# Kernel tuning notes

Measured on AMD Instinct MI355X. Metric: run time of the kernel, lower is better.

## Reference

```python
import jax, jax.numpy as jnp
import numpy as np

N_NODES = 50000
N_EDGES = 400000
D_IN = 2048
D_OUT = 512


def setup_inputs() -> dict:
    key = jax.random.key(0)
    k1, k2, k3 = jax.random.split(key, 3)
    x = jax.random.normal(k1, (N_NODES, D_IN), dtype=jnp.float32)
    edge_index = jax.random.randint(k2, (2, N_EDGES), 0, N_NODES, dtype=jnp.int64)
    # Glorot init like PyG GCNConv
    scale = jnp.sqrt(6.0 / (D_IN + D_OUT)).astype(jnp.float32)
    weight = jax.random.uniform(k3, (D_IN, D_OUT), dtype=jnp.float32, minval=-scale, maxval=scale)
    bias = jnp.zeros((D_OUT,), dtype=jnp.float32)
    return {"x": x, "edge_index": edge_index, "weight": weight, "bias": bias}


def reference(x, edge_index, weight, bias):
    N = x.shape[0]
    # GCNConv(normalize=True): add self-loops, symmetric deg^-1/2 normalization
    loops = jnp.arange(N, dtype=edge_index.dtype)
    src = jnp.concatenate([edge_index[0], loops])  # message sources (x_j)
    dst = jnp.concatenate([edge_index[1], loops])  # aggregation targets
    ones = jnp.ones(dst.shape[0], dtype=x.dtype)
    deg = jax.ops.segment_sum(ones, dst, num_segments=N)  # [N]
    deg_inv_sqrt = jnp.where(deg > 0, jax.lax.rsqrt(deg), 0.0)
    norm = deg_inv_sqrt[src] * deg_inv_sqrt[dst]  # [E+N]
    h = x @ weight  # [N, d_out] linear transform before propagation
    msgs = norm[:, None] * h[src]  # [E+N, d_out]
    out = jax.ops.segment_sum(msgs, dst, num_segments=N) + bias  # [N, d_out]
    return jax.nn.log_softmax(out, axis=1)
```

## Files before the change

### kernel.cpp

```cpp
#include <hip/hip_runtime.h>
#include <stdint.h>

#define D_IN   2048
#define D_OUT  512

typedef __bf16 bf16;
typedef bf16     bf16x8 __attribute__((ext_vector_type(8)));
typedef float    f32x4  __attribute__((ext_vector_type(4)));
typedef uint32_t u32x4  __attribute__((ext_vector_type(4)));

#define GLP(p)  (const __attribute__((address_space(1))) void*)(p)
#define LDSP(p) (__attribute__((address_space(3))) void*)(p)

__global__ void k_count(const int* __restrict__ dstv, int* __restrict__ cnt, int E) {
    int e = blockIdx.x * blockDim.x + threadIdx.x;
    if (e < E) atomicAdd(&cnt[dstv[e]], 1);
}

__global__ __launch_bounds__(1024) void k_scan1(const int* __restrict__ cnt,
                                                int* __restrict__ offs,
                                                int* __restrict__ bsum,
                                                float* __restrict__ dis,
                                                int* __restrict__ cur, int n) {
    __shared__ int wsum[16], wbase[16];
    const int tid = threadIdx.x, lane = tid & 63, wv = tid >> 6;
    int i = blockIdx.x * 1024 + tid;
    int v = (i < n) ? cnt[i] : 0;
    int x = v;
    #pragma unroll
    for (int d = 1; d < 64; d <<= 1) {
        int y = __shfl_up(x, d);
        if (lane >= d) x += y;
    }
    if (lane == 63) wsum[wv] = x;
    __syncthreads();
    if (tid < 16) {
        int s = 0;
        for (int j = 0; j < tid; ++j) s += wsum[j];
        wbase[tid] = s;
    }
    __syncthreads();
    if (i < n) {
        offs[i] = wbase[wv] + x - v;
        dis[i]  = rsqrtf((float)(v + 1));
        cur[i]  = 0;
    }
    if (tid == 0) bsum[blockIdx.x] = wbase[15] + wsum[15];
}

__global__ void k_scan2(int* __restrict__ bsum, int nb) {
    int t = threadIdx.x;
    if (nb <= 64) {
        int v = (t < nb) ? bsum[t] : 0;
        int x = v;
        #pragma unroll
        for (int d = 1; d < 64; d <<= 1) {
            int y = __shfl_up(x, d);
            if (t >= d) x += y;
        }
        if (t < nb) bsum[t] = x - v;
    } else if (t == 0) {
        int run = 0;
        for (int j = 0; j < nb; ++j) { int v = bsum[j]; bsum[j] = run; run += v; }
    }
}

__global__ void k_fill(const int* __restrict__ srcv, const int* __restrict__ dstv,
                       const int* __restrict__ offs, const int* __restrict__ bsum,
                       int* __restrict__ cur, int* __restrict__ csr, int E) {
    int e = blockIdx.x * blockDim.x + threadIdx.x;
    if (e < E) {
        int d = dstv[e];
        int p = offs[d] + bsum[d >> 10] + atomicAdd(&cur[d], 1);
        csr[p] = srcv[e];
    }
}

__global__ void k_wt(const float* __restrict__ W, uint16_t* __restrict__ wt) {
    __shared__ float t[32][33];
    int kb = blockIdx.x * 32, nb = blockIdx.y * 32;
    int tx = threadIdx.x, ty = threadIdx.y;
    #pragma unroll
    for (int i = 0; i < 32; i += 8)
        t[ty + i][tx] = W[(size_t)(kb + ty + i) * D_OUT + nb + tx];
    __syncthreads();
    bf16* o = (bf16*)wt;
    #pragma unroll
    for (int i = 0; i < 32; i += 8)
        o[(size_t)(nb + ty + i) * D_IN + kb + tx] = (bf16)t[tx][ty + i];
}

__global__ __launch_bounds__(256, 2) void k_gemm(const float* __restrict__ X,
                                                 const uint16_t* __restrict__ WT,
                                                 uint16_t* __restrict__ H, int M) {
    __shared__ uint16_t lsA[2][128 * 64];
    __shared__ uint16_t lsB[2][128 * 64];
    const int nwg = gridDim.x;
    const int b = blockIdx.x;
    const int q = nwg >> 3, r = nwg & 7;
    const int xcd = b & 7, lo = b >> 3;
    const int g = (xcd < r) ? (xcd * (q + 1) + lo) : (r * (q + 1) + (xcd - r) * q + lo);
    const int m0 = (g >> 2) * 128;
    const int n0 = (g & 3) * 128;
    const int tid = threadIdx.x;
    const int w = tid >> 6, lane = tid & 63;
    const int wr = w >> 1, wc = w & 1;
    const int lr = lane & 15, lk = lane >> 4;
    const int NT = D_IN / 64;

    f32x4 acc[4][4];
    #pragma unroll
    for (int m = 0; m < 4; m++)
        #pragma unroll
        for (int n = 0; n < 4; n++) acc[m][n] = (f32x4)(0.0f);

    const float* aSrc[4];
    int aDst[4];
    const uint16_t* bSrc[4];
    #pragma unroll
    for (int j = 0; j < 4; j++) {
        int uidx = (w * 4 + j) * 64 + lane;
        int row = uidx >> 3, u = uidx & 7;
        int lrow = row;
        if (m0 + row >= M) lrow = (M - 1) - m0;
        aSrc[j] = X + (size_t)(m0 + lrow) * D_IN + u * 8;
        aDst[j] = row * 64 + (u ^ (row & 7)) * 8;
        bSrc[j] = WT + (size_t)(n0 + row) * D_IN + (u ^ (row & 7)) * 8;
    }

    f32x4 set0[8], set1[8];

    auto loadA = [&](f32x4* s, int t) {
        t &= (NT - 1);
        #pragma unroll
        for (int j = 0; j < 4; j++) {
            s[2 * j]     = *(const f32x4*)(aSrc[j] + t * 64);
            s[2 * j + 1] = *(const f32x4*)(aSrc[j] + t * 64 + 4);
        }
    };
    auto writeA = [&](const f32x4* s, int buf) {
        #pragma unroll
        for (int j = 0; j < 4; j++) {
            f32x4 a0 = s[2 * j], a1 = s[2 * j + 1];
            bf16x8 tv;
            tv[0] = (bf16)a0[0]; tv[1] = (bf16)a0[1]; tv[2] = (bf16)a0[2]; tv[3] = (bf16)a0[3];
            tv[4] = (bf16)a1[0]; tv[5] = (bf16)a1[1]; tv[6] = (bf16)a1[2]; tv[7] = (bf16)a1[3];
            *(bf16x8*)(&lsA[buf][aDst[j]]) = tv;
        }
    };
    auto stageB = [&](int t, int buf) {
        t &= (NT - 1);
        #pragma unroll
        for (int j = 0; j < 4; j++)
            __builtin_amdgcn_global_load_lds(GLP(bSrc[j] + t * 64),
                                             LDSP(&lsB[buf][(w * 4 + j) * 512]), 16, 0, 0);
    };
    auto compute = [&](int buf) {
        #pragma unroll
        for (int kk = 0; kk < 2; kk++) {
            bf16x8 aF[4], bF[4];
            #pragma unroll
            for (int m = 0; m < 4; m++) {
                int row = wr * 64 + m * 16 + lr;
                aF[m] = *(const bf16x8*)(&lsA[buf][row * 64 + (((kk * 4 + lk) ^ (row & 7)) * 8)]);
            }
            #pragma unroll
            for (int n = 0; n < 4; n++) {
                int row = wc * 64 + n * 16 + lr;
                bF[n] = *(const bf16x8*)(&lsB[buf][row * 64 + (((kk * 4 + lk) ^ (row & 7)) * 8)]);
            }
            #pragma unroll
            for (int m = 0; m < 4; m++)
                #pragma unroll
                for (int n = 0; n < 4; n++)
                    acc[m][n] = __builtin_amdgcn_mfma_f32_16x16x32_bf16(aF[m], bF[n], acc[m][n], 0, 0, 0);
        }
    };

    loadA(set0, 0);
    stageB(0, 0);
    loadA(set1, 1);
    asm volatile("s_waitcnt vmcnt(12)" ::: "memory");
    writeA(set0, 0);

    #pragma unroll 1
    for (int t = 0; t < NT; t += 2) {
        stageB(t + 1, 1);
        loadA(set0, t + 2);
        asm volatile("s_waitcnt vmcnt(12)" ::: "memory");
        writeA(set1, 1);
        asm volatile("s_waitcnt lgkmcnt(0)" ::: "memory");
        __builtin_amdgcn_s_barrier();
        compute(0);
        __builtin_amdgcn_s_barrier();
        stageB(t + 2, 0);
        loadA(set1, t + 3);
        asm volatile("s_waitcnt vmcnt(12)" ::: "memory");
        writeA(set0, 0);
        asm volatile("s_waitcnt lgkmcnt(0)" ::: "memory");
        __builtin_amdgcn_s_barrier();
        compute(1);
        __builtin_amdgcn_s_barrier();
    }
    asm volatile("s_waitcnt vmcnt(0)" ::: "memory");

    #pragma unroll
    for (int m = 0; m < 4; m++) {
        int rbase = m0 + wr * 64 + m * 16 + lk * 4;
        #pragma unroll
        for (int n = 0; n < 4; n++) {
            int col = n0 + wc * 64 + n * 16 + lr;
            #pragma unroll
            for (int j = 0; j < 4; j++) {
                int row = rbase + j;
                if (row < M) {
                    bf16 tv = (bf16)acc[m][n][j];
                    H[(size_t)row * D_OUT + col] = __builtin_bit_cast(uint16_t, tv);
                }
            }
        }
    }
}

__global__ __launch_bounds__(256) void k_agg(const uint16_t* __restrict__ h,
                                             const int* __restrict__ csr,
                                             const int* __restrict__ offs,
                                             const int* __restrict__ bsum,
                                             const int* __restrict__ cnt,
                                             const float* __restrict__ dis,
                                             const float* __restrict__ bias,
                                             float* __restrict__ out, int N) {
    const int wv = threadIdx.x >> 6, lane = threadIdx.x & 63;
    const int i = blockIdx.x * 4 + wv;
    if (i >= N) return;
    const float di = dis[i];
    float acc[8];
    {
        u32x4 v = *(const u32x4*)(h + (size_t)i * D_OUT + lane * 8);
        float s2 = di * di;
        #pragma unroll
        for (int k = 0; k < 4; k++) {
            acc[2 * k]     = __builtin_bit_cast(float, v[k] << 16) * s2;
            acc[2 * k + 1] = __builtin_bit_cast(float, v[k] & 0xffff0000u) * s2;
        }
    }
    const int o = offs[i] + bsum[i >> 10], c = cnt[i];
    for (int e = o; e < o + c; ++e) {
        int s = csr[e];
        float ws = di * dis[s];
        u32x4 v = *(const u32x4*)(h + (size_t)s * D_OUT + lane * 8);
        #pragma unroll
        for (int k = 0; k < 4; k++) {
            acc[2 * k]     += __builtin_bit_cast(float, v[k] << 16) * ws;
            acc[2 * k + 1] += __builtin_bit_cast(float, v[k] & 0xffff0000u) * ws;
        }
    }
    {
        const f32x4* bp = (const f32x4*)(bias + lane * 8);
        f32x4 b0 = bp[0], b1 = bp[1];
        #pragma unroll
        for (int k = 0; k < 4; k++) { acc[k] += b0[k]; acc[4 + k] += b1[k]; }
    }
    float mx = acc[0];
    #pragma unroll
    for (int k = 1; k < 8; k++) mx = fmaxf(mx, acc[k]);
    #pragma unroll
    for (int d = 1; d < 64; d <<= 1) mx = fmaxf(mx, __shfl_xor(mx, d));
    float se = 0.f;
    #pragma unroll
    for (int k = 0; k < 8; k++) se += expf(acc[k] - mx);
    #pragma unroll
    for (int d = 1; d < 64; d <<= 1) se += __shfl_xor(se, d);
    float lse = mx + logf(se);
    f32x4 o0, o1;
    #pragma unroll
    for (int k = 0; k < 4; k++) { o0[k] = acc[k] - lse; o1[k] = acc[4 + k] - lse; }
    f32x4* op = (f32x4*)(out + (size_t)i * D_OUT + lane * 8);
    op[0] = o0; op[1] = o1;
}

extern "C" void kernel_launch(void* const* d_in, const int* in_sizes, int n_in,
                              void* d_out, int out_size, void* d_ws, size_t ws_size,
                              hipStream_t stream) {
    const float* x    = (const float*)d_in[0];
    const int*   ei   = (const int*)d_in[1];
    const float* W    = (const float*)d_in[2];
    const float* bias = (const float*)d_in[3];
    float* out = (float*)d_out;

    const int N = in_sizes[0] / D_IN;
    const int E = in_sizes[1] / 2;
    const int* srcv = ei;
    const int* dstv = ei + E;

    char* p = (char*)d_ws;
    auto carve = [&](size_t b) { void* r = (void*)p; p += (b + 255) & ~(size_t)255; return r; };
    uint16_t* h    = (uint16_t*)carve((size_t)N * D_OUT * 2);
    uint16_t* wt   = (uint16_t*)carve((size_t)D_OUT * D_IN * 2);
    int*      cnt  = (int*)carve((size_t)N * 4);
    int*      cur  = (int*)carve((size_t)N * 4);
    float*    dis  = (float*)carve((size_t)N * 4);
    int*      offs = (int*)carve((size_t)N * 4);
    int*      csr  = (int*)carve((size_t)E * 4);
    int*      bsum = (int*)carve(1024 * 4);

    hipMemsetAsync(cnt, 0, (size_t)N * 4, stream);

    k_wt<<<dim3(D_IN / 32, D_OUT / 32), dim3(32, 8), 0, stream>>>(W, wt);
    k_count<<<(E + 255) / 256, 256, 0, stream>>>(dstv, cnt, E);
    const int nb = (N + 1023) / 1024;
    k_scan1<<<nb, 1024, 0, stream>>>(cnt, offs, bsum, dis, cur, N);
    k_scan2<<<1, 64, 0, stream>>>(bsum, nb);
    k_fill<<<(E + 255) / 256, 256, 0, stream>>>(srcv, dstv, offs, bsum, cur, csr, E);

    k_gemm<<<((N + 127) / 128) * 4, 256, 0, stream>>>(x, wt, h, N);

    k_agg<<<(N + 3) / 4, 256, 0, stream>>>(h, csr, offs, bsum, cnt, dis, bias, out, N);
}
```

Before: 358.9 us.

## Restructure GEMM pipeline for higher occupancy, precompute edge norms, unroll aggregation

The GEMM drops the double-buffered A tile and the second register set, and raises the occupancy hint to 3 blocks per CU. It reorders the loop so A's global loads for the next step overlap the current compute. k_fill now stores each edge's source deg^-1/2 alongside the CSR entry, so the aggregation skips a dependent gather from dis. The aggregation loop is unrolled by 4 so four neighbour rows are loaded at once, increasing memory-level parallelism. Risks include A-load latency being exposed with less buffering, register spills under the tighter launch bound, and an extra E-sized array write.

```diff
diff --git a/kernel.cpp b/kernel.cpp
--- a/kernel.cpp
+++ b/kernel.cpp
@@ -67,12 +67,15 @@
 
 __global__ void k_fill(const int* __restrict__ srcv, const int* __restrict__ dstv,
                        const int* __restrict__ offs, const int* __restrict__ bsum,
-                       int* __restrict__ cur, int* __restrict__ csr, int E) {
+                       const float* __restrict__ dis, int* __restrict__ cur,
+                       int* __restrict__ csr, float* __restrict__ nrm, int E) {
     int e = blockIdx.x * blockDim.x + threadIdx.x;
     if (e < E) {
         int d = dstv[e];
+        int s = srcv[e];
         int p = offs[d] + bsum[d >> 10] + atomicAdd(&cur[d], 1);
-        csr[p] = srcv[e];
+        csr[p] = s;
+        nrm[p] = dis[s];
     }
 }
 
@@ -90,10 +93,10 @@
         o[(size_t)(nb + ty + i) * D_IN + kb + tx] = (bf16)t[tx][ty + i];
 }
 
-__global__ __launch_bounds__(256, 2) void k_gemm(const float* __restrict__ X,
+__global__ __launch_bounds__(256, 3) void k_gemm(const float* __restrict__ X,
                                                  const uint16_t* __restrict__ WT,
                                                  uint16_t* __restrict__ H, int M) {
-    __shared__ uint16_t lsA[2][128 * 64];
+    __shared__ uint16_t lsA[128 * 64];
     __shared__ uint16_t lsB[2][128 * 64];
     const int nwg = gridDim.x;
     const int b = blockIdx.x;
@@ -128,24 +131,24 @@
         bSrc[j] = WT + (size_t)(n0 + row) * D_IN + (u ^ (row & 7)) * 8;
     }
 
-    f32x4 set0[8], set1[8];
-
-    auto loadA = [&](f32x4* s, int t) {
+    f32x4 ar[8];
+
+    auto loadA = [&](int t) {
         t &= (NT - 1);
         #pragma unroll
         for (int j = 0; j < 4; j++) {
-            s[2 * j]     = *(const f32x4*)(aSrc[j] + t * 64);
-            s[2 * j + 1] = *(const f32x4*)(aSrc[j] + t * 64 + 4);
+            ar[2 * j]     = *(const f32x4*)(aSrc[j] + t * 64);
+            ar[2 * j + 1] = *(const f32x4*)(aSrc[j] + t * 64 + 4);
         }
     };
-    auto writeA = [&](const f32x4* s, int buf) {
+    auto writeA = [&]() {
         #pragma unroll
         for (int j = 0; j < 4; j++) {
-            f32x4 a0 = s[2 * j], a1 = s[2 * j + 1];
+            f32x4 a0 = ar[2 * j], a1 = ar[2 * j + 1];
             bf16x8 tv;
             tv[0] = (bf16)a0[0]; tv[1] = (bf16)a0[1]; tv[2] = (bf16)a0[2]; tv[3] = (bf16)a0[3];
             tv[4] = (bf16)a1[0]; tv[5] = (bf16)a1[1]; tv[6] = (bf16)a1[2]; tv[7] = (bf16)a1[3];
-            *(bf16x8*)(&lsA[buf][aDst[j]]) = tv;
+            *(bf16x8*)(&lsA[aDst[j]]) = tv;
         }
     };
     auto stageB = [&](int t, int buf) {
@@ -162,7 +165,7 @@
             #pragma unroll
             for (int m = 0; m < 4; m++) {
                 int row = wr * 64 + m * 16 + lr;
-                aF[m] = *(const bf16x8*)(&lsA[buf][row * 64 + (((kk * 4 + lk) ^ (row & 7)) * 8)]);
+                aF[m] = *(const bf16x8*)(&lsA[row * 64 + (((kk * 4 + lk) ^ (row & 7)) * 8)]);
             }
             #pragma unroll
             for (int n = 0; n < 4; n++) {
@@ -177,29 +180,32 @@
         }
     };
 
-    loadA(set0, 0);
+    loadA(0);
     stageB(0, 0);
-    loadA(set1, 1);
-    asm volatile("s_waitcnt vmcnt(12)" ::: "memory");
-    writeA(set0, 0);
+    stageB(1, 1);
+    asm volatile("s_waitcnt vmcnt(8)" ::: "memory");
+    writeA();
+    asm volatile("s_waitcnt vmcnt(4)" ::: "memory");
+    asm volatile("s_waitcnt lgkmcnt(0)" ::: "memory");
+    __builtin_amdgcn_s_barrier();
 
     #pragma unroll 1
     for (int t = 0; t < NT; t += 2) {
-        stageB(t + 1, 1);
-        loadA(set0, t + 2);
-        asm volatile("s_waitcnt vmcnt(12)" ::: "memory");
-        writeA(set1, 1);
-        asm volatile("s_waitcnt lgkmcnt(0)" ::: "memory");
-        __builtin_amdgcn_s_barrier();
+        loadA(t + 1);
         compute(0);
         __builtin_amdgcn_s_barrier();
         stageB(t + 2, 0);
-        loadA(set1, t + 3);
-        asm volatile("s_waitcnt vmcnt(12)" ::: "memory");
-        writeA(set0, 0);
+        asm volatile("s_waitcnt vmcnt(4)" ::: "memory");
+        writeA();
         asm volatile("s_waitcnt lgkmcnt(0)" ::: "memory");
         __builtin_amdgcn_s_barrier();
+        loadA(t + 2);
         compute(1);
+        __builtin_amdgcn_s_barrier();
+        stageB(t + 3, 1);
+        asm volatile("s_waitcnt vmcnt(4)" ::: "memory");
+        writeA();
+        asm volatile("s_waitcnt lgkmcnt(0)" ::: "memory");
         __builtin_amdgcn_s_barrier();
     }
     asm volatile("s_waitcnt vmcnt(0)" ::: "memory");
@@ -224,6 +230,7 @@
 
 __global__ __launch_bounds__(256) void k_agg(const uint16_t* __restrict__ h,
                                              const int* __restrict__ csr,
+                                             const float* __restrict__ nrm,
                                              const int* __restrict__ offs,
                                              const int* __restrict__ bsum,
                                              const int* __restrict__ cnt,
@@ -244,15 +251,36 @@
             acc[2 * k + 1] = __builtin_bit_cast(float, v[k] & 0xffff0000u) * s2;
         }
     }
-    const int o = offs[i] + bsum[i >> 10], c = cnt[i];
-    for (int e = o; e < o + c; ++e) {
-        int s = csr[e];
-        float ws = di * dis[s];
-        u32x4 v = *(const u32x4*)(h + (size_t)s * D_OUT + lane * 8);
+    const int o = offs[i] + bsum[i >> 10], cend = o + cnt[i];
+    int e = o;
+    for (; e + 4 <= cend; e += 4) {
+        int s0 = csr[e], s1 = csr[e + 1], s2 = csr[e + 2], s3 = csr[e + 3];
+        float w0 = di * nrm[e],     w1 = di * nrm[e + 1];
+        float w2 = di * nrm[e + 2], w3 = di * nrm[e + 3];
+        u32x4 v0 = *(const u32x4*)(h + (size_t)s0 * D_OUT + lane * 8);
+        u32x4 v1 = *(const u32x4*)(h + (size_t)s1 * D_OUT + lane * 8);
+        u32x4 v2 = *(const u32x4*)(h + (size_t)s2 * D_OUT + lane * 8);
+        u32x4 v3 = *(const u32x4*)(h + (size_t)s3 * D_OUT + lane * 8);
         #pragma unroll
         for (int k = 0; k < 4; k++) {
-            acc[2 * k]     += __builtin_bit_cast(float, v[k] << 16) * ws;
-            acc[2 * k + 1] += __builtin_bit_cast(float, v[k] & 0xffff0000u) * ws;
+            acc[2 * k]     += __builtin_bit_cast(float, v0[k] << 16) * w0
+                            + __builtin_bit_cast(float, v1[k] << 16) * w1
+                            + __builtin_bit_cast(float, v2[k] << 16) * w2
+                            + __builtin_bit_cast(float, v3[k] << 16) * w3;
+            acc[2 * k + 1] += __builtin_bit_cast(float, v0[k] & 0xffff0000u) * w0
+                            + __builtin_bit_cast(float, v1[k] & 0xffff0000u) * w1
+                            + __builtin_bit_cast(float, v2[k] & 0xffff0000u) * w2
+                            + __builtin_bit_cast(float, v3[k] & 0xffff0000u) * w3;
+        }
+    }
+    for (; e < cend; ++e) {
+        int s0 = csr[e];
+        float w0 = di * nrm[e];
+        u32x4 v0 = *(const u32x4*)(h + (size_t)s0 * D_OUT + lane * 8);
+        #pragma unroll
+        for (int k = 0; k < 4; k++) {
+            acc[2 * k]     += __builtin_bit_cast(float, v0[k] << 16) * w0;
+            acc[2 * k + 1] += __builtin_bit_cast(float, v0[k] & 0xffff0000u) * w0;
         }
     }
     {
@@ -302,6 +330,7 @@
     float*    dis  = (float*)carve((size_t)N * 4);
     int*      offs = (int*)carve((size_t)N * 4);
     int*      csr  = (int*)carve((size_t)E * 4);
+    float*    nrm  = (float*)carve((size_t)E * 4);
     int*      bsum = (int*)carve(1024 * 4);
 
     hipMemsetAsync(cnt, 0, (size_t)N * 4, stream);
@@ -311,9 +340,9 @@
     const int nb = (N + 1023) / 1024;
     k_scan1<<<nb, 1024, 0, stream>>>(cnt, offs, bsum, dis, cur, N);
     k_scan2<<<1, 64, 0, stream>>>(bsum, nb);
-    k_fill<<<(E + 255) / 256, 256, 0, stream>>>(srcv, dstv, offs, bsum, cur, csr, E);
+    k_fill<<<(E + 255) / 256, 256, 0, stream>>>(srcv, dstv, offs, bsum, dis, cur, csr, nrm, E);
 
     k_gemm<<<((N + 127) / 128) * 4, 256, 0, stream>>>(x, wt, h, N);
 
-    k_agg<<<(N + 3) / 4, 256, 0, stream>>>(h, csr, offs, bsum, cnt, dis, bias, out, N);
-}
+    k_agg<<<(N + 3) / 4, 256, 0, stream>>>(h, csr, nrm, offs, bsum, cnt, dis, bias, out, N);
+}
```

After: 349.7 us. 2.6% less time.
